# Kernel tuning notes

Measured on AMD Instinct MI355X. Metric: run time of the kernel, lower is better.

Reference implementation:

```python
import jax, jax.numpy as jnp
import numpy as np

DIM = 1024
HEADS = 16
HEAD_DIM = DIM // HEADS
SCALE = HEAD_DIM ** -0.5
EPS = 1e-5


def _ln(x, g, b):
    m = jnp.mean(x, axis=-1, keepdims=True)
    v = jnp.mean((x - m) ** 2, axis=-1, keepdims=True)
    return (x - m) * jax.lax.rsqrt(v + EPS) * g + b


def setup_inputs() -> dict:
    key = jax.random.key(0)
    ks = jax.random.split(key, 12)
    B, N, C = 4, 1024, DIM
    s = lambda fan: 1.0 / np.sqrt(fan)
    return {
        "src_q": jax.random.normal(ks[0], (B, N, C), jnp.float32),
        "src_kv": jax.random.normal(ks[1], (B, N, C), jnp.float32),
        "gq": jnp.ones((C,), jnp.float32), "bq": jnp.zeros((C,), jnp.float32),
        "gkv": jnp.ones((C,), jnp.float32), "bkv": jnp.zeros((C,), jnp.float32),
        "Wq": jax.random.normal(ks[2], (C, C), jnp.float32) * s(C),
        "Wkv": jax.random.normal(ks[3], (C, 2 * C), jnp.float32) * s(C),
        "Wproj": jax.random.normal(ks[4], (C, C), jnp.float32) * s(C),
        "bproj": jnp.zeros((C,), jnp.float32),
        "gn": jnp.ones((C,), jnp.float32), "bn": jnp.zeros((C,), jnp.float32),
        "W1": jax.random.normal(ks[5], (C, 4 * C), jnp.float32) * s(C),
        "b1": jnp.zeros((4 * C,), jnp.float32),
        "W2": jax.random.normal(ks[6], (4 * C, C), jnp.float32) * s(4 * C),
        "b2": jnp.zeros((C,), jnp.float32),
    }


def reference(src_q, src_kv, gq, bq, gkv, bkv, Wq, Wkv, Wproj, bproj,
              gn, bn, W1, b1, W2, b2):
    B, N, C = src_q.shape
    qn = _ln(src_q, gq, bq)
    kvn = _ln(src_kv, gkv, bkv)
    # Q: [B, H, N, d]
    Q = (qn @ Wq).reshape(B, N, HEADS, HEAD_DIM).transpose(0, 2, 1, 3)
    KV = (kvn @ Wkv).reshape(B, N, 2, HEADS, HEAD_DIM).transpose(2, 0, 3, 1, 4)
    K, V = KV[0], KV[1]
    attn = jnp.einsum('bhqd,bhkd->bhqk', Q, K) * SCALE
    attn = jax.nn.softmax(attn, axis=-1)
    # NOTE: original code multiplies by scale a second time here (faithful)
    x = jnp.einsum('bhqk,bhkd->bhqd', attn, V) * SCALE
    x = x.transpose(0, 2, 1, 3).reshape(B, N, C)
    x = x @ Wproj + bproj
    src = src_q + x               # residual (drop_path = identity in eval)
    src = _ln(src, gn, bn)
    h = jax.nn.gelu(src @ W1 + b1, approximate=False)
    src2 = h @ W2 + b2
    return src + src2
```

## Files before the change

kernel.cpp:

```cpp
#include <hip/hip_runtime.h>
#include <hip/hip_bf16.h>
#include <math.h>

typedef __bf16 bf16;
typedef __bf16 bf16x2 __attribute__((ext_vector_type(2)));
typedef __bf16 bf16x8 __attribute__((ext_vector_type(8)));
typedef float f32x4 __attribute__((ext_vector_type(4)));
typedef float f32x16 __attribute__((ext_vector_type(16)));
typedef unsigned int u32;
typedef unsigned int u32x2 __attribute__((ext_vector_type(2)));
typedef unsigned int u32x4 __attribute__((ext_vector_type(4)));

#define SCALE 0.125f

#define GLOAD_LDS16(gptr, lptr)                                      \
  __builtin_amdgcn_global_load_lds(                                  \
      (const __attribute__((address_space(1))) void*)(gptr),         \
      (__attribute__((address_space(3))) void*)(lptr), 16, 0, 0)

template <int N>
__device__ __forceinline__ void vmcnt_wait() {
  if constexpr (N == 0) asm volatile("s_waitcnt vmcnt(0)" ::: "memory");
  else if constexpr (N == 4) asm volatile("s_waitcnt vmcnt(4)" ::: "memory");
  else if constexpr (N == 6) asm volatile("s_waitcnt vmcnt(6)" ::: "memory");
  else static_assert(N == 0 || N == 4 || N == 6, "unsupported vmcnt");
}

__device__ __forceinline__ void xcd_swz(int gx, int gy, int& x, int& y) {
  int w = blockIdx.x + gx * blockIdx.y;
  int nwg = gx * gy;
  int wp = (w & 7) * (nwg >> 3) + (w >> 3);
  int xi = wp & 7;
  int t = wp >> 3;
  y = t % gy;
  x = (t / gy) * 8 + xi;
}

__device__ __forceinline__ u32 pk_bf16(float lo, float hi) {
  bf16x2 t;
  t[0] = (bf16)lo;
  t[1] = (bf16)hi;
  return __builtin_bit_cast(u32, t);
}

__device__ __forceinline__ void plane32_swap(u32& a, u32& b) {
  asm volatile("v_permlane32_swap_b32 %0, %1" : "+v"(a), "+v"(b));
}

__global__ __launch_bounds__(256) void ln_f32(const float* __restrict__ x,
                                              const float* __restrict__ g,
                                              const float* __restrict__ b,
                                              bf16* __restrict__ y) {
  long base = (long)blockIdx.x * 1024;
  int tid = threadIdx.x;
  float v[4];
#pragma unroll
  for (int i = 0; i < 4; i++) v[i] = x[base + tid + i * 256];
  float s1 = v[0] + v[1] + v[2] + v[3];
  float s2 = v[0] * v[0] + v[1] * v[1] + v[2] * v[2] + v[3] * v[3];
#pragma unroll
  for (int off = 32; off; off >>= 1) {
    s1 += __shfl_xor(s1, off);
    s2 += __shfl_xor(s2, off);
  }
  __shared__ float aux[2][4];
  int wave = tid >> 6, lane = tid & 63;
  if (lane == 0) { aux[0][wave] = s1; aux[1][wave] = s2; }
  __syncthreads();
  float S1 = aux[0][0] + aux[0][1] + aux[0][2] + aux[0][3];
  float S2 = aux[1][0] + aux[1][1] + aux[1][2] + aux[1][3];
  float mean = S1 * (1.0f / 1024.0f);
  float var = S2 * (1.0f / 1024.0f) - mean * mean;
  float rs = rsqrtf(var + 1e-5f);
#pragma unroll
  for (int i = 0; i < 4; i++) {
    int c = tid + i * 256;
    y[base + c] = (bf16)(((v[i] - mean) * rs) * g[c] + b[c]);
  }
}

__global__ __launch_bounds__(256) void transpose_w(const float* __restrict__ W,
                                                   bf16* __restrict__ Wt,
                                                   int K, int N) {
  __shared__ bf16 tile[64][66];
  int n0 = blockIdx.x * 64, k0 = blockIdx.y * 64;
  int c = threadIdx.x & 63, r4 = threadIdx.x >> 6;
#pragma unroll
  for (int i = 0; i < 16; i++)
    tile[i * 4 + r4][c] = (bf16)W[(long)(k0 + i * 4 + r4) * N + n0 + c];
  __syncthreads();
#pragma unroll
  for (int i = 0; i < 16; i++)
    Wt[(long)(n0 + i * 4 + r4) * K + k0 + c] = tile[c][i * 4 + r4];
}

__global__ __launch_bounds__(256) void extract_vt(const bf16* __restrict__ KV,
                                                  bf16* __restrict__ Vt) {
  __shared__ bf16 tile[64][66];
  int bh = blockIdx.z, b = bh >> 4, h = bh & 15;
  const bf16* src = KV + (long)b * 1024 * 2048 + 1024 + h * 64;
  bf16* dst = Vt + (long)bh * 64 * 1024;
  int n0 = blockIdx.x * 64;
  int c = threadIdx.x & 63, r4 = threadIdx.x >> 6;
#pragma unroll
  for (int i = 0; i < 16; i++)
    tile[i * 4 + r4][c] = src[(long)(n0 + i * 4 + r4) * 2048 + c];
  __syncthreads();
#pragma unroll
  for (int i = 0; i < 16; i++)
    dst[(long)(i * 4 + r4) * 1024 + n0 + c] = tile[c][i * 4 + r4];
}

__global__ __launch_bounds__(256) void attn_fused(
    const bf16* __restrict__ Q,
    const bf16* __restrict__ KV,
    const bf16* __restrict__ Vt,
    bf16* __restrict__ X) {
  __shared__ __align__(16) bf16 Qs[128 * 64];
  __shared__ __align__(16) bf16 Ks[2][64 * 128];
  __shared__ __align__(16) bf16 Vs[2][64 * 128];
  int tid = threadIdx.x, wave = tid >> 6, lane = tid & 63;
  int l31 = lane & 31, h = lane >> 5;
  int bqx, bhy;
  xcd_swz(8, 64, bqx, bhy);
  int bh = bhy, b = bh >> 4, hd = bh & 15;
  const bf16* Qb = Q + (long)b * 1048576 + hd * 64;
  const bf16* Kb = KV + (long)b * 2097152 + hd * 64;
  const bf16* Vb = Vt + (long)bh * 65536;
  bf16* Xb = X + (long)b * 1048576 + hd * 64;
  int q0 = bqx * 128;

  const bf16* gk[4];
  const bf16* gv[4];
  int eoKV[4];
#pragma unroll
  for (int t = 0; t < 4; t++) {
    int eo = (t * 256 + tid) * 8;
    eoKV[t] = eo;
    int r2 = eo >> 7, pp = (eo & 127) >> 3, q = pp ^ (r2 & 15);
    gk[t] = &Kb[(long)(r2 + ((q >> 3) << 6)) * 2048 + ((q & 7) << 3)];
    gv[t] = &Vb[(long)r2 * 1024 + (q << 3)];
  }

#pragma unroll
  for (int t = 0; t < 4; t++) {
    int eo = (t * 256 + tid) * 8;
    int r = eo >> 6, p = (eo & 63) >> 3;
    int c = (p ^ (r & 7)) << 3;
    GLOAD_LDS16(&Qb[(long)(q0 + r) * 1024 + c], &Qs[eo]);
  }
#pragma unroll
  for (int t = 0; t < 4; t++) GLOAD_LDS16(gk[t], &Ks[0][eoKV[t]]);
#pragma unroll
  for (int t = 0; t < 4; t++) GLOAD_LDS16(gv[t], &Vs[0][eoKV[t]]);
  __syncthreads();

  bf16x8 qf[4];
  {
    int r = wave * 32 + l31;
#pragma unroll
    for (int dw = 0; dw < 4; dw++) {
      int p = (dw * 2 + h) ^ (r & 7);
      qf[dw] = *(const bf16x8*)&Qs[r * 64 + p * 8];
    }
  }

  const float C = 0.18033688011112042f;
  float m_run = -1e30f, l_run = 0.0f;
  f32x16 acc[2] = {};
  int cur = 0;

  for (int kc = 0; kc < 8; kc++) {
    if (kc < 7) {
#pragma unroll
      for (int t = 0; t < 4; t++)
        GLOAD_LDS16(gk[t] + (long)(kc + 1) * 128 * 2048, &Ks[cur ^ 1][eoKV[t]]);
#pragma unroll
      for (int t = 0; t < 4; t++)
        GLOAD_LDS16(gv[t] + (kc + 1) * 128, &Vs[cur ^ 1][eoKV[t]]);
    }
    const bf16* ks = Ks[cur];
    const bf16* vs = Vs[cur];

    f32x16 s[4] = {};
#pragma unroll
    for (int kt = 0; kt < 4; kt++) {
      int k = kt * 32 + l31;
      int r2 = k & 63, hi = k >> 6;
#pragma unroll
      for (int dw = 0; dw < 4; dw++) {
        int p = (hi * 8 + dw * 2 + h) ^ (r2 & 15);
        bf16x8 kf = *(const bf16x8*)&ks[r2 * 128 + p * 8];
        s[kt] = __builtin_amdgcn_mfma_f32_32x32x16_bf16(kf, qf[dw], s[kt], 0, 0, 0);
      }
    }

    float mk[4];
#pragma unroll
    for (int kt = 0; kt < 4; kt++) {
      float m01 = fmaxf(fmaxf(s[kt][0], s[kt][1]), fmaxf(s[kt][2], s[kt][3]));
      float m23 = fmaxf(fmaxf(s[kt][4], s[kt][5]), fmaxf(s[kt][6], s[kt][7]));
      float m45 = fmaxf(fmaxf(s[kt][8], s[kt][9]), fmaxf(s[kt][10], s[kt][11]));
      float m67 = fmaxf(fmaxf(s[kt][12], s[kt][13]), fmaxf(s[kt][14], s[kt][15]));
      mk[kt] = fmaxf(fmaxf(m01, m23), fmaxf(m45, m67));
    }
    float mx = fmaxf(fmaxf(mk[0], mk[1]), fmaxf(mk[2], mk[3]));
    mx = fmaxf(mx, __shfl_xor(mx, 32));
    float m_new = fmaxf(m_run, mx);
    float alpha = exp2f((m_run - m_new) * C);
    m_run = m_new;
    float mc = m_new * C;
    float rk[4];
#pragma unroll
    for (int kt = 0; kt < 4; kt++) {
      float r0 = 0.0f;
#pragma unroll
      for (int r = 0; r < 16; r++) {
        float pv = exp2f(s[kt][r] * C - mc);
        s[kt][r] = pv;
        r0 += pv;
      }
      rk[kt] = r0;
    }
    float rs = (rk[0] + rk[1]) + (rk[2] + rk[3]);
    rs += __shfl_xor(rs, 32);
    l_run = l_run * alpha + rs;
#pragma unroll
    for (int nt = 0; nt < 2; nt++)
#pragma unroll
      for (int r = 0; r < 16; r++) acc[nt][r] *= alpha;

#pragma unroll
    for (int kw = 0; kw < 8; kw++) {
      int kt = kw >> 1, rb = (kw & 1) * 8;
      u32 wA = pk_bf16(s[kt][rb + 0], s[kt][rb + 1]);
      u32 wB = pk_bf16(s[kt][rb + 2], s[kt][rb + 3]);
      u32 wC = pk_bf16(s[kt][rb + 4], s[kt][rb + 5]);
      u32 wD = pk_bf16(s[kt][rb + 6], s[kt][rb + 7]);
      plane32_swap(wA, wC);
      plane32_swap(wB, wD);
      u32x4 wv = {wA, wB, wC, wD};
      bf16x8 pf = __builtin_bit_cast(bf16x8, wv);
#pragma unroll
      for (int nt = 0; nt < 2; nt++) {
        int r2 = nt * 32 + l31;
        int p = (kw * 2 + h) ^ (r2 & 15);
        bf16x8 vf = *(const bf16x8*)&vs[r2 * 128 + p * 8];
        acc[nt] = __builtin_amdgcn_mfma_f32_32x32x16_bf16(vf, pf, acc[nt], 0, 0, 0);
      }
    }

    if (kc < 7) {
      __syncthreads();
      cur ^= 1;
    }
  }

  float fs = SCALE / l_run;
  bf16* Os = Qs;
  int qrow = wave * 32 + l31;
#pragma unroll
  for (int nt = 0; nt < 2; nt++)
#pragma unroll
    for (int g = 0; g < 4; g++) {
      u32 w0 = pk_bf16(acc[nt][g * 4 + 0] * fs, acc[nt][g * 4 + 1] * fs);
      u32 w1 = pk_bf16(acc[nt][g * 4 + 2] * fs, acc[nt][g * 4 + 3] * fs);
      int s8 = nt * 8 + g * 2 + h;
      int phys = s8 ^ (qrow & 15);
      u32x2 wv = {w0, w1};
      *(u32x2*)&Os[qrow * 64 + phys * 4] = wv;
    }
  int rrow = wave * 32 + (lane >> 1);
  int cbase = (lane & 1) * 32;
#pragma unroll
  for (int t2 = 0; t2 < 4; t2++) {
    int s0 = (lane & 1) * 8 + t2 * 2;
    u32x2 a = *(u32x2*)&Os[rrow * 64 + ((s0 ^ (rrow & 15)) * 4)];
    u32x2 bb = *(u32x2*)&Os[rrow * 64 + (((s0 + 1) ^ (rrow & 15)) * 4)];
    u32x4 o4 = {a[0], a[1], bb[0], bb[1]};
    *(u32x4*)&Xb[(long)(q0 + rrow) * 1024 + cbase + t2 * 8] = o4;
  }
}

template <int BM, int BN, int WR, int WC, int EPI, int CF32, int RBF16>
__global__ __launch_bounds__(512) void gemm_p(
    const bf16* __restrict__ A, int lda,
    const bf16* __restrict__ B, int ldb,
    void* __restrict__ Cv, int ldc, int K,
    const float* __restrict__ bias,
    const void* __restrict__ resv, int ldr) {
  constexpr int MT = BM / (16 * WR);
  constexpr int NT = BN / (16 * WC);
  constexpr int L = (BM + BN) / 64;
  constexpr int LA = BM / 64;
  constexpr int AE = BM * 64;
  constexpr int BUFE = (BM + BN) * 64;
  __shared__ __align__(16) bf16 lds[3 * BUFE];
  int tid = threadIdx.x;
  int wave = tid >> 6, lane = tid & 63;
  int wm = wave / WC, wn = wave % WC;
  int quad = lane >> 4, l16 = lane & 15;
  int bx, by;
  xcd_swz(gridDim.x, gridDim.y, bx, by);
  int m0 = by * BM, n0 = bx * BN;

  const bf16* gp[L];
  int lo[L];
#pragma unroll
  for (int i = 0; i < L; i++) {
    if (i < LA) {
      int eo = (i * 512 + tid) * 8;
      int r = eo >> 6, p = (eo & 63) >> 3;
      int c = (p ^ (r & 7)) << 3;
      gp[i] = &A[(long)(m0 + r) * lda + c];
      lo[i] = eo;
    } else {
      int eo = ((i - LA) * 512 + tid) * 8;
      int r = eo >> 6, p = (eo & 63) >> 3;
      int c = (p ^ (r & 7)) << 3;
      gp[i] = &B[(long)(n0 + r) * ldb + c];
      lo[i] = AE + eo;
    }
  }

  int ntk = K >> 6;
#pragma unroll
  for (int i = 0; i < L; i++) GLOAD_LDS16(gp[i], &lds[lo[i]]);
#pragma unroll
  for (int i = 0; i < L; i++) gp[i] += 64;
#pragma unroll
  for (int i = 0; i < L; i++) GLOAD_LDS16(gp[i], &lds[BUFE + lo[i]]);
#pragma unroll
  for (int i = 0; i < L; i++) gp[i] += 64;
  vmcnt_wait<L>();
  asm volatile("" ::: "memory");
  __builtin_amdgcn_s_barrier();

  f32x4 acc[MT][NT] = {};
  int b = 0;
  for (int t = 0; t < ntk; t++) {
    const bf16* Al = &lds[b * BUFE];
    const bf16* Bl = &lds[b * BUFE + AE];
    int b2 = b + 2; if (b2 >= 3) b2 -= 3;
    bool more = (t + 2) < ntk;

    bf16x8 af[2][MT], bv[2][NT];
#pragma unroll
    for (int ks = 0; ks < 2; ks++) {
#pragma unroll
      for (int mt = 0; mt < MT; mt++) {
        int row = wm * (BM / WR) + mt * 16 + l16;
        int p = (ks * 4 + quad) ^ (row & 7);
        af[ks][mt] = *(const bf16x8*)&Al[row * 64 + p * 8];
      }
#pragma unroll
      for (int nt = 0; nt < NT; nt++) {
        int row = wn * (BN / WC) + nt * 16 + l16;
        int p = (ks * 4 + quad) ^ (row & 7);
        bv[ks][nt] = *(const bf16x8*)&Bl[row * 64 + p * 8];
      }
    }
    if (more) {
#pragma unroll
      for (int i = 0; i < L; i++) GLOAD_LDS16(gp[i], &lds[b2 * BUFE + lo[i]]);
    }
    asm volatile("s_waitcnt lgkmcnt(0)" ::: "memory");
    __builtin_amdgcn_sched_barrier(0);
    __builtin_amdgcn_s_setprio(1);
#pragma unroll
    for (int ks = 0; ks < 2; ks++)
#pragma unroll
      for (int mt = 0; mt < MT; mt++)
#pragma unroll
        for (int nt = 0; nt < NT; nt++)
          acc[mt][nt] = __builtin_amdgcn_mfma_f32_16x16x32_bf16(
              af[ks][mt], bv[ks][nt], acc[mt][nt], 0, 0, 0);
    __builtin_amdgcn_s_setprio(0);
    __builtin_amdgcn_sched_barrier(0);
    if (more) {
      vmcnt_wait<L>();
    } else if (t + 1 < ntk) {
      vmcnt_wait<0>();
    }
    if (t + 1 < ntk) {
      asm volatile("" ::: "memory");
      __builtin_amdgcn_s_barrier();
    }
#pragma unroll
    for (int i = 0; i < L; i++) gp[i] += 64;
    b += 1; if (b == 3) b = 0;
  }

  int gm = m0 + wm * (BM / WR), gn = n0 + wn * (BN / WC);
#pragma unroll
  for (int nt = 0; nt < NT; nt++) {
    int col = gn + nt * 16 + l16;
    float bvb = (EPI != 0) ? bias[col] : 0.0f;
#pragma unroll
    for (int mt = 0; mt < MT; mt++) {
#pragma unroll
      for (int r = 0; r < 4; r++) {
        int row = gm + mt * 16 + quad * 4 + r;
        float v = acc[mt][nt][r] + bvb;
        if (EPI == 2) {
          v = 0.5f * v * (1.0f + erff(v * 0.70710678118654752f));
        } else if (EPI == 1) {
          float rv = RBF16 ? (float)((const bf16*)resv)[(long)row * ldr + col]
                           : ((const float*)resv)[(long)row * ldr + col];
          v += rv;
        }
        if (CF32)
          ((float*)Cv)[(long)row * ldc + col] = v;
        else
          ((bf16*)Cv)[(long)row * ldc + col] = (bf16)v;
      }
    }
  }
}

template <int EPI, int CF32, int RBF16>
__global__ __launch_bounds__(256, 2) void gemm_d(
    const bf16* __restrict__ A, int lda,
    const bf16* __restrict__ B, int ldb,
    void* __restrict__ Cv, int ldc, int K,
    const float* __restrict__ bias,
    const void* __restrict__ resv, int ldr) {
  constexpr int AE = 128 * 64;
  constexpr int BUFE = 256 * 64;
  __shared__ __align__(16) bf16 lds[2 * BUFE];
  int tid = threadIdx.x;
  int wave = tid >> 6, lane = tid & 63;
  int wm = wave >> 1, wn = wave & 1;
  int quad = lane >> 4, l16 = lane & 15;
  int bx, by;
  xcd_swz(gridDim.x, gridDim.y, bx, by);
  int m0 = by * 128, n0 = bx * 128;

  const bf16* gp[8];
  int lo[8];
#pragma unroll
  for (int i = 0; i < 8; i++) {
    if (i < 4) {
      int eo = (i * 256 + tid) * 8;
      int r = eo >> 6, p = (eo & 63) >> 3;
      int c = (p ^ (r & 7)) << 3;
      gp[i] = &A[(long)(m0 + r) * lda + c];
      lo[i] = eo;
    } else {
      int eo = ((i - 4) * 256 + tid) * 8;
      int r = eo >> 6, p = (eo & 63) >> 3;
      int c = (p ^ (r & 7)) << 3;
      gp[i] = &B[(long)(n0 + r) * ldb + c];
      lo[i] = AE + eo;
    }
  }

  int ntk = K >> 6;
#pragma unroll
  for (int i = 0; i < 8; i++) GLOAD_LDS16(gp[i], &lds[lo[i]]);
#pragma unroll
  for (int i = 0; i < 8; i++) gp[i] += 64;
  vmcnt_wait<0>();
  asm volatile("" ::: "memory");
  __builtin_amdgcn_s_barrier();

  f32x4 acc[4][4] = {};
  for (int t = 0; t < ntk; t++) {
    const bf16* Al = &lds[(t & 1) * BUFE];
    const bf16* Bl = &lds[(t & 1) * BUFE + AE];
    if (t + 1 < ntk) {
#pragma unroll
      for (int i = 0; i < 8; i++)
        GLOAD_LDS16(gp[i], &lds[((t + 1) & 1) * BUFE + lo[i]]);
#pragma unroll
      for (int i = 0; i < 8; i++) gp[i] += 64;
    }
    bf16x8 af[2][4], bv[2][4];
#pragma unroll
    for (int ks = 0; ks < 2; ks++) {
#pragma unroll
      for (int mt = 0; mt < 4; mt++) {
        int row = wm * 64 + mt * 16 + l16;
        int p = (ks * 4 + quad) ^ (row & 7);
        af[ks][mt] = *(const bf16x8*)&Al[row * 64 + p * 8];
      }
#pragma unroll
      for (int nt = 0; nt < 4; nt++) {
        int row = wn * 64 + nt * 16 + l16;
        int p = (ks * 4 + quad) ^ (row & 7);
        bv[ks][nt] = *(const bf16x8*)&Bl[row * 64 + p * 8];
      }
    }
    asm volatile("s_waitcnt lgkmcnt(0)" ::: "memory");
    __builtin_amdgcn_sched_barrier(0);
    __builtin_amdgcn_s_setprio(1);
#pragma unroll
    for (int ks = 0; ks < 2; ks++)
#pragma unroll
      for (int mt = 0; mt < 4; mt++)
#pragma unroll
        for (int nt = 0; nt < 4; nt++)
          acc[mt][nt] = __builtin_amdgcn_mfma_f32_16x16x32_bf16(
              af[ks][mt], bv[ks][nt], acc[mt][nt], 0, 0, 0);
    __builtin_amdgcn_s_setprio(0);
    __builtin_amdgcn_sched_barrier(0);
    if (t + 1 < ntk) {
      vmcnt_wait<0>();
      asm volatile("" ::: "memory");
      __builtin_amdgcn_s_barrier();
    }
  }

  int gm = m0 + wm * 64, gn = n0 + wn * 64;
#pragma unroll
  for (int nt = 0; nt < 4; nt++) {
    int col = gn + nt * 16 + l16;
    float bvb = (EPI != 0) ? bias[col] : 0.0f;
#pragma unroll
    for (int mt = 0; mt < 4; mt++) {
#pragma unroll
      for (int r = 0; r < 4; r++) {
        int row = gm + mt * 16 + quad * 4 + r;
        float v = acc[mt][nt][r] + bvb;
        if (EPI == 2) {
          v = 0.5f * v * (1.0f + erff(v * 0.70710678118654752f));
        } else if (EPI == 1) {
          float rv = RBF16 ? (float)((const bf16*)resv)[(long)row * ldr + col]
                           : ((const float*)resv)[(long)row * ldr + col];
          v += rv;
        }
        if (CF32)
          ((float*)Cv)[(long)row * ldc + col] = v;
        else
          ((bf16*)Cv)[(long)row * ldc + col] = (bf16)v;
      }
    }
  }
}

extern "C" void kernel_launch(void* const* d_in, const int* in_sizes, int n_in,
                              void* d_out, int out_size, void* d_ws, size_t ws_size,
                              hipStream_t stream) {
  const float* src_q  = (const float*)d_in[0];
  const float* src_kv = (const float*)d_in[1];
  const float* gq     = (const float*)d_in[2];
  const float* bq     = (const float*)d_in[3];
  const float* gkv    = (const float*)d_in[4];
  const float* bkv    = (const float*)d_in[5];
  const float* Wq     = (const float*)d_in[6];
  const float* Wkv    = (const float*)d_in[7];
  const float* Wproj  = (const float*)d_in[8];
  const float* bproj  = (const float*)d_in[9];
  const float* gn     = (const float*)d_in[10];
  const float* bn     = (const float*)d_in[11];
  const float* W1     = (const float*)d_in[12];
  const float* b1     = (const float*)d_in[13];
  const float* W2     = (const float*)d_in[14];
  const float* b2     = (const float*)d_in[15];
  float* out = (float*)d_out;

  char* ws = (char*)d_ws;
  const long MB = 1024 * 1024;
  bf16* Wq_t    = (bf16*)(ws + 0 * MB);
  bf16* Wkv_t   = (bf16*)(ws + 2 * MB);
  bf16* Wproj_t = (bf16*)(ws + 6 * MB);
  bf16* W1_t    = (bf16*)(ws + 8 * MB);
  bf16* W2_t    = (bf16*)(ws + 16 * MB);
  bf16* qn      = (bf16*)(ws + 24 * MB);
  bf16* kvn     = (bf16*)(ws + 32 * MB);
  bf16* Qm      = (bf16*)(ws + 40 * MB);
  bf16* KVm     = (bf16*)(ws + 48 * MB);
  bf16* Vt      = (bf16*)(ws + 64 * MB);
  bf16* xbuf    = (bf16*)(ws + 24 * MB);
  float* tbuf   = (float*)(ws + 48 * MB);
  bf16* sbuf    = (bf16*)(ws + 64 * MB);
  bf16* hbuf    = (bf16*)(ws + 72 * MB);

  transpose_w<<<dim3(16, 16), 256, 0, stream>>>(Wq, Wq_t, 1024, 1024);
  transpose_w<<<dim3(32, 16), 256, 0, stream>>>(Wkv, Wkv_t, 1024, 2048);
  transpose_w<<<dim3(16, 16), 256, 0, stream>>>(Wproj, Wproj_t, 1024, 1024);
  transpose_w<<<dim3(64, 16), 256, 0, stream>>>(W1, W1_t, 1024, 4096);
  transpose_w<<<dim3(16, 64), 256, 0, stream>>>(W2, W2_t, 4096, 1024);

  ln_f32<<<4096, 256, 0, stream>>>(src_q, gq, bq, qn);
  ln_f32<<<4096, 256, 0, stream>>>(src_kv, gkv, bkv, kvn);

  gemm_p<128, 128, 2, 4, 0, 0, 0><<<dim3(8, 32), 512, 0, stream>>>(
      qn, 1024, Wq_t, 1024, Qm, 1024, 1024, nullptr, nullptr, 0);
  gemm_d<0, 0, 0><<<dim3(16, 32), 256, 0, stream>>>(
      kvn, 1024, Wkv_t, 1024, KVm, 2048, 1024, nullptr, nullptr, 0);
  extract_vt<<<dim3(16, 1, 64), 256, 0, stream>>>(KVm, Vt);

  attn_fused<<<dim3(8, 64), 256, 0, stream>>>(Qm, KVm, Vt, xbuf);

  gemm_p<128, 128, 2, 4, 1, 1, 0><<<dim3(8, 32), 512, 0, stream>>>(
      xbuf, 1024, Wproj_t, 1024, tbuf, 1024, 1024, bproj, src_q, 1024);
  ln_f32<<<4096, 256, 0, stream>>>(tbuf, gn, bn, sbuf);
  gemm_d<2, 0, 0><<<dim3(32, 32), 256, 0, stream>>>(
      sbuf, 1024, W1_t, 1024, hbuf, 4096, 1024, b1, nullptr, 0);
  gemm_p<128, 128, 2, 4, 1, 1, 1><<<dim3(8, 32), 512, 0, stream>>>(
      hbuf, 4096, W2_t, 4096, out, 1024, 4096, b2, sbuf, 1024);
}
```

Before: 358.1 us.

## Merge weight transposes and input layernorms into one prologue; fuse V transpose into KV GEMM

```diff
diff --git a/kernel.cpp b/kernel.cpp
--- a/kernel.cpp
+++ b/kernel.cpp
@@ -4,6 +4,7 @@
 
 typedef __bf16 bf16;
 typedef __bf16 bf16x2 __attribute__((ext_vector_type(2)));
+typedef __bf16 bf16x4 __attribute__((ext_vector_type(4)));
 typedef __bf16 bf16x8 __attribute__((ext_vector_type(8)));
 typedef float f32x4 __attribute__((ext_vector_type(4)));
 typedef float f32x16 __attribute__((ext_vector_type(16)));
@@ -45,6 +46,74 @@
 
 __device__ __forceinline__ void plane32_swap(u32& a, u32& b) {
   asm volatile("v_permlane32_swap_b32 %0, %1" : "+v"(a), "+v"(b));
+}
+
+__global__ __launch_bounds__(256) void prologue(
+    const float* __restrict__ Wq, const float* __restrict__ Wkv,
+    const float* __restrict__ Wproj, const float* __restrict__ W1,
+    const float* __restrict__ W2,
+    bf16* __restrict__ Wq_t, bf16* __restrict__ Wkv_t,
+    bf16* __restrict__ Wproj_t, bf16* __restrict__ W1_t,
+    bf16* __restrict__ W2_t,
+    const float* __restrict__ src_q, const float* __restrict__ src_kv,
+    const float* __restrict__ gq, const float* __restrict__ bq,
+    const float* __restrict__ gkv, const float* __restrict__ bkv,
+    bf16* __restrict__ qn, bf16* __restrict__ kvn) {
+  __shared__ bf16 tile[64][66];
+  __shared__ float aux[2][4];
+  int id = blockIdx.x;
+  int tid = threadIdx.x;
+  if (id < 3072) {
+    const float* W;
+    bf16* Wt;
+    int K, N, base, tx;
+    if (id < 256)       { W = Wq;    Wt = Wq_t;    K = 1024; N = 1024; base = 0;    tx = 16; }
+    else if (id < 768)  { W = Wkv;   Wt = Wkv_t;   K = 1024; N = 2048; base = 256;  tx = 32; }
+    else if (id < 1024) { W = Wproj; Wt = Wproj_t; K = 1024; N = 1024; base = 768;  tx = 16; }
+    else if (id < 2048) { W = W1;    Wt = W1_t;    K = 1024; N = 4096; base = 1024; tx = 64; }
+    else                { W = W2;    Wt = W2_t;    K = 4096; N = 1024; base = 2048; tx = 16; }
+    int lid = id - base;
+    int n0 = (lid % tx) * 64, k0 = (lid / tx) * 64;
+    int c = tid & 63, r4 = tid >> 6;
+#pragma unroll
+    for (int i = 0; i < 16; i++)
+      tile[i * 4 + r4][c] = (bf16)W[(long)(k0 + i * 4 + r4) * N + n0 + c];
+    __syncthreads();
+#pragma unroll
+    for (int i = 0; i < 16; i++)
+      Wt[(long)(n0 + i * 4 + r4) * K + k0 + c] = tile[c][i * 4 + r4];
+  } else {
+    int lid = id - 3072;
+    bool isq = lid < 4096;
+    const float* x = isq ? src_q : src_kv;
+    const float* g = isq ? gq : gkv;
+    const float* b = isq ? bq : bkv;
+    bf16* y = isq ? qn : kvn;
+    long base = (long)(lid & 4095) * 1024;
+    float v[4];
+#pragma unroll
+    for (int i = 0; i < 4; i++) v[i] = x[base + tid + i * 256];
+    float s1 = v[0] + v[1] + v[2] + v[3];
+    float s2 = v[0] * v[0] + v[1] * v[1] + v[2] * v[2] + v[3] * v[3];
+#pragma unroll
+    for (int off = 32; off; off >>= 1) {
+      s1 += __shfl_xor(s1, off);
+      s2 += __shfl_xor(s2, off);
+    }
+    int wave = tid >> 6, lane = tid & 63;
+    if (lane == 0) { aux[0][wave] = s1; aux[1][wave] = s2; }
+    __syncthreads();
+    float S1 = aux[0][0] + aux[0][1] + aux[0][2] + aux[0][3];
+    float S2 = aux[1][0] + aux[1][1] + aux[1][2] + aux[1][3];
+    float mean = S1 * (1.0f / 1024.0f);
+    float var = S2 * (1.0f / 1024.0f) - mean * mean;
+    float rs = rsqrtf(var + 1e-5f);
+#pragma unroll
+    for (int i = 0; i < 4; i++) {
+      int c = tid + i * 256;
+      y[base + c] = (bf16)(((v[i] - mean) * rs) * g[c] + b[c]);
+    }
+  }
 }
 
 __global__ __launch_bounds__(256) void ln_f32(const float* __restrict__ x,
@@ -77,38 +146,6 @@
     int c = tid + i * 256;
     y[base + c] = (bf16)(((v[i] - mean) * rs) * g[c] + b[c]);
   }
-}
-
-__global__ __launch_bounds__(256) void transpose_w(const float* __restrict__ W,
-                                                   bf16* __restrict__ Wt,
-                                                   int K, int N) {
-  __shared__ bf16 tile[64][66];
-  int n0 = blockIdx.x * 64, k0 = blockIdx.y * 64;
-  int c = threadIdx.x & 63, r4 = threadIdx.x >> 6;
-#pragma unroll
-  for (int i = 0; i < 16; i++)
-    tile[i * 4 + r4][c] = (bf16)W[(long)(k0 + i * 4 + r4) * N + n0 + c];
-  __syncthreads();
-#pragma unroll
-  for (int i = 0; i < 16; i++)
-    Wt[(long)(n0 + i * 4 + r4) * K + k0 + c] = tile[c][i * 4 + r4];
-}
-
-__global__ __launch_bounds__(256) void extract_vt(const bf16* __restrict__ KV,
-                                                  bf16* __restrict__ Vt) {
-  __shared__ bf16 tile[64][66];
-  int bh = blockIdx.z, b = bh >> 4, h = bh & 15;
-  const bf16* src = KV + (long)b * 1024 * 2048 + 1024 + h * 64;
-  bf16* dst = Vt + (long)bh * 64 * 1024;
-  int n0 = blockIdx.x * 64;
-  int c = threadIdx.x & 63, r4 = threadIdx.x >> 6;
-#pragma unroll
-  for (int i = 0; i < 16; i++)
-    tile[i * 4 + r4][c] = src[(long)(n0 + i * 4 + r4) * 2048 + c];
-  __syncthreads();
-#pragma unroll
-  for (int i = 0; i < 16; i++)
-    dst[(long)(i * 4 + r4) * 1024 + n0 + c] = tile[c][i * 4 + r4];
 }
 
 __global__ __launch_bounds__(256) void attn_fused(
@@ -515,9 +552,10 @@
 #pragma unroll
   for (int nt = 0; nt < 4; nt++) {
     int col = gn + nt * 16 + l16;
-    float bvb = (EPI != 0) ? bias[col] : 0.0f;
+    float bvb = (EPI == 1 || EPI == 2) ? bias[col] : 0.0f;
 #pragma unroll
     for (int mt = 0; mt < 4; mt++) {
+      bf16 vt4[4];
 #pragma unroll
       for (int r = 0; r < 4; r++) {
         int row = gm + mt * 16 + quad * 4 + r;
@@ -529,10 +567,22 @@
                            : ((const float*)resv)[(long)row * ldr + col];
           v += rv;
         }
+        bf16 hv = (bf16)v;
         if (CF32)
           ((float*)Cv)[(long)row * ldc + col] = v;
         else
-          ((bf16*)Cv)[(long)row * ldc + col] = (bf16)v;
+          ((bf16*)Cv)[(long)row * ldc + col] = hv;
+        vt4[r] = hv;
+      }
+      if (EPI == 3 && col >= 1024) {
+        int row0 = gm + mt * 16 + quad * 4;
+        int bb = row0 >> 10, n = row0 & 1023;
+        int hcol = col - 1024;
+        bf16* Vt = (bf16*)resv;
+        long vo = ((long)(bb * 16 + (hcol >> 6))) * 65536 + (long)(hcol & 63) * 1024 + n;
+        bf16x4 pk4;
+        pk4[0] = vt4[0]; pk4[1] = vt4[1]; pk4[2] = vt4[2]; pk4[3] = vt4[3];
+        *(bf16x4*)&Vt[vo] = pk4;
       }
     }
   }
@@ -576,20 +626,14 @@
   bf16* sbuf    = (bf16*)(ws + 64 * MB);
   bf16* hbuf    = (bf16*)(ws + 72 * MB);
 
-  transpose_w<<<dim3(16, 16), 256, 0, stream>>>(Wq, Wq_t, 1024, 1024);
-  transpose_w<<<dim3(32, 16), 256, 0, stream>>>(Wkv, Wkv_t, 1024, 2048);
-  transpose_w<<<dim3(16, 16), 256, 0, stream>>>(Wproj, Wproj_t, 1024, 1024);
-  transpose_w<<<dim3(64, 16), 256, 0, stream>>>(W1, W1_t, 1024, 4096);
-  transpose_w<<<dim3(16, 64), 256, 0, stream>>>(W2, W2_t, 4096, 1024);
-
-  ln_f32<<<4096, 256, 0, stream>>>(src_q, gq, bq, qn);
-  ln_f32<<<4096, 256, 0, stream>>>(src_kv, gkv, bkv, kvn);
+  prologue<<<11264, 256, 0, stream>>>(
+      Wq, Wkv, Wproj, W1, W2, Wq_t, Wkv_t, Wproj_t, W1_t, W2_t,
+      src_q, src_kv, gq, bq, gkv, bkv, qn, kvn);
 
   gemm_p<128, 128, 2, 4, 0, 0, 0><<<dim3(8, 32), 512, 0, stream>>>(
       qn, 1024, Wq_t, 1024, Qm, 1024, 1024, nullptr, nullptr, 0);
-  gemm_d<0, 0, 0><<<dim3(16, 32), 256, 0, stream>>>(
-      kvn, 1024, Wkv_t, 1024, KVm, 2048, 1024, nullptr, nullptr, 0);
-  extract_vt<<<dim3(16, 1, 64), 256, 0, stream>>>(KVm, Vt);
+  gemm_d<3, 0, 0><<<dim3(16, 32), 256, 0, stream>>>(
+      kvn, 1024, Wkv_t, 1024, KVm, 2048, 1024, nullptr, Vt, 0);
 
   attn_fused<<<dim3(8, 64), 256, 0, stream>>>(Qm, KVm, Vt, xbuf);
 
```

Measured after the change: 338.6 us. 1.06x faster.
